# Optimization experiments

Hardware: AMD Instinct MI355X
Metric: run time of the kernel (lower is better)

## Reference

```python
import jax, jax.numpy as jnp
import numpy as np

NUM_NODES = 5000
NUM_COLORS = 20
NODE_FEAT = 4
COLOR_FEAT = 3
COMBINED = NODE_FEAT + COLOR_FEAT  # 7
HIDDEN = 128
N_GRAPH = NUM_NODES * NUM_COLORS   # 100000 GCN nodes (batch=1)
N_EDGES = 1_600_000


def setup_inputs() -> dict:
    key = jax.random.key(0)
    ks = jax.random.split(key, 12)
    flat_obs = jax.random.normal(ks[0], (1, 3 + NUM_NODES * NODE_FEAT + NUM_COLORS * COLOR_FEAT), dtype=jnp.float32)
    edge_index = jax.random.randint(ks[1], (2, N_EDGES), 0, N_GRAPH, dtype=jnp.int64)
    s = lambda k, sh, fan: jax.random.normal(k, sh, dtype=jnp.float32) / np.sqrt(fan)
    return {
        "flat_obs": flat_obs,
        "edge_index": edge_index,
        "W1": s(ks[2], (COMBINED, HIDDEN), COMBINED),
        "b1": jnp.zeros((HIDDEN,), jnp.float32),
        "W2": s(ks[3], (HIDDEN, HIDDEN), HIDDEN),
        "b2": jnp.zeros((HIDDEN,), jnp.float32),
        "fc1_w": s(ks[4], (HIDDEN, HIDDEN), HIDDEN),
        "fc1_b": jnp.zeros((HIDDEN,), jnp.float32),
        "fc2_w": s(ks[5], (HIDDEN, 1), HIDDEN),
        "fc2_b": jnp.zeros((1,), jnp.float32),
    }


def _gcn_conv(x, W, b, src, dst, norm):
    # PyG GCNConv: out[dst] += norm * (x @ W)[src]; self-loops already in src/dst.
    xw = x @ W                                   # [N, H]
    msg = xw[src] * norm[:, None]                # [E+N, H]
    out = jax.ops.segment_sum(msg, dst, num_segments=N_GRAPH)
    return out + b


def reference(flat_obs, edge_index, W1, b1, W2, b2, fc1_w, fc1_b, fc2_w, fc2_b):
    B = flat_obs.shape[0]
    nf_start = 3
    nf_end = nf_start + NUM_NODES * NODE_FEAT
    cf_end = nf_end + NUM_COLORS * COLOR_FEAT
    node_features = flat_obs[:, nf_start:nf_end].reshape(B, NUM_NODES, NODE_FEAT)
    color_features = flat_obs[:, nf_end:cf_end].reshape(B, NUM_COLORS, COLOR_FEAT)

    # cross-expand: [B, nodes, colors, 4+3]
    en = jnp.broadcast_to(node_features[:, :, None, :], (B, NUM_NODES, NUM_COLORS, NODE_FEAT))
    ec = jnp.broadcast_to(color_features[:, None, :, :], (B, NUM_NODES, NUM_COLORS, COLOR_FEAT))
    combined = jnp.concatenate([en, ec], axis=3).reshape(-1, COMBINED)  # [N_GRAPH, 7]

    # add self loops + symmetric normalization (GCN)
    loops = jnp.arange(N_GRAPH, dtype=edge_index.dtype)
    src = jnp.concatenate([edge_index[0], loops])
    dst = jnp.concatenate([edge_index[1], loops])
    deg = jax.ops.segment_sum(jnp.ones_like(dst, dtype=jnp.float32), dst, num_segments=N_GRAPH)
    dinv = jnp.where(deg > 0, jax.lax.rsqrt(deg), 0.0)
    norm = dinv[src] * dinv[dst]

    x = jax.nn.relu(_gcn_conv(combined, W1, b1, src, dst, norm))
    x = jax.nn.relu(_gcn_conv(x, W2, b2, src, dst, norm))
    x = jax.nn.relu(x @ fc1_w + fc1_b)
    q = x @ fc2_w + fc2_b                         # [N_GRAPH, 1]
    return q.reshape(B, NUM_NODES * NUM_COLORS)
```

## Files before the change

### kernel.cpp

```cpp
#include <hip/hip_runtime.h>
#include <hip/hip_fp16.h>

#define NGRAPH 100000
#define NEDGE  1600000
#define HID    128
#define SCAN_B 512
#define NBLK   ((NGRAPH + SCAN_B - 1) / SCAN_B)
#define TILE   64

__device__ __forceinline__ int e_src(const int* ei, int is64, int e) {
    return is64 ? ei[2 * e] : ei[e];
}
__device__ __forceinline__ int e_dst(const int* ei, int is64, int e) {
    return is64 ? ei[2 * NEDGE + 2 * e] : ei[NEDGE + e];
}

__global__ void k_prep(const float* __restrict__ obs, const int* __restrict__ ei,
                       float* __restrict__ comb, int* __restrict__ deg,
                       int* __restrict__ fill, int* __restrict__ flag) {
    if (blockIdx.x == 0 && threadIdx.x < 64) {
        int v = ei[2 * threadIdx.x + 1];
        unsigned long long b = __ballot(v != 0);
        if (threadIdx.x == 0) flag[0] = (b == 0ull) ? 1 : 0;
    }
    int i = blockIdx.x * blockDim.x + threadIdx.x;
    if (i >= NGRAPH) return;
    int n = i / 20, c = i % 20;
    const float* nf = obs + 3 + n * 4;
    const float* cf = obs + 3 + 20000 + c * 3;
    float* o = comb + i * 7;
    o[0] = nf[0]; o[1] = nf[1]; o[2] = nf[2]; o[3] = nf[3];
    o[4] = cf[0]; o[5] = cf[1]; o[6] = cf[2];
    deg[i] = 0;
    fill[i] = 0;
}

__global__ void k_deg(const int* __restrict__ ei, const int* __restrict__ flag,
                      int* __restrict__ deg) {
    int e = blockIdx.x * blockDim.x + threadIdx.x;
    if (e >= NEDGE) return;
    atomicAdd(&deg[e_dst(ei, flag[0], e)], 1);
}

__global__ void __launch_bounds__(SCAN_B) k_scan1(const int* __restrict__ deg,
                                                  int* __restrict__ rowptr,
                                                  int* __restrict__ sums,
                                                  float* __restrict__ dinv) {
    __shared__ int sh[SCAN_B];
    int t = threadIdx.x;
    int i = blockIdx.x * SCAN_B + t;
    int val = (i < NGRAPH) ? deg[i] : 0;
    if (i < NGRAPH) dinv[i] = rsqrtf((float)(val + 1));
    sh[t] = val;
    __syncthreads();
    for (int o = 1; o < SCAN_B; o <<= 1) {
        int x = (t >= o) ? sh[t - o] : 0;
        __syncthreads();
        sh[t] += x;
        __syncthreads();
    }
    if (i < NGRAPH) rowptr[i] = sh[t] - val;
    if (t == SCAN_B - 1) sums[blockIdx.x] = sh[t];
}

__global__ void __launch_bounds__(256) k_scan2(int* __restrict__ sums) {
    __shared__ int sh[256];
    int t = threadIdx.x;
    int val = (t < NBLK) ? sums[t] : 0;
    sh[t] = val;
    __syncthreads();
    for (int o = 1; o < 256; o <<= 1) {
        int x = (t >= o) ? sh[t - o] : 0;
        __syncthreads();
        sh[t] += x;
        __syncthreads();
    }
    if (t < NBLK) sums[t] = sh[t] - val;
}

__global__ void __launch_bounds__(SCAN_B) k_scan3(int* __restrict__ rowptr,
                                                  const int* __restrict__ sums) {
    int i = blockIdx.x * SCAN_B + threadIdx.x;
    if (i < NGRAPH) rowptr[i] += sums[blockIdx.x];
}

__global__ void k_fill(const int* __restrict__ ei, const int* __restrict__ flag,
                       const float* __restrict__ dinv,
                       const int* __restrict__ rowptr, int* __restrict__ fill,
                       int2* __restrict__ csr) {
    int e = blockIdx.x * blockDim.x + threadIdx.x;
    if (e >= NEDGE) return;
    int is64 = flag[0];
    int s = e_src(ei, is64, e);
    int d = e_dst(ei, is64, e);
    int pos = rowptr[d] + atomicAdd(&fill[d], 1);
    csr[pos] = make_int2(s, __float_as_int(dinv[s] * dinv[d]));
}

__global__ void __launch_bounds__(256) k_gcn1(const int* __restrict__ rowptr,
                                              const int* __restrict__ deg,
                                              const int2* __restrict__ csr,
                                              const float* __restrict__ dinv,
                                              const float* __restrict__ comb,
                                              const float* __restrict__ W1,
                                              const float* __restrict__ b1,
                                              __half* __restrict__ x1) {
    __shared__ float agg_s[32][8];
    int g = threadIdx.x >> 3;
    int f = threadIdx.x & 7;
    int d = blockIdx.x * 32 + g;
    if (f < 7) {
        int start = rowptr[d], n = deg[d];
        float acc = 0.0f;
        for (int j = 0; j < n; ++j) {
            int2 ed = csr[start + j];
            acc += __int_as_float(ed.y) * comb[ed.x * 7 + f];
        }
        float dv = dinv[d];
        acc += dv * dv * comb[d * 7 + f];
        agg_s[g][f] = acc;
    }
    __syncthreads();
    float a[7];
    #pragma unroll
    for (int q = 0; q < 7; ++q) a[q] = agg_s[g][q];
    int h0 = f * 16;
    #pragma unroll
    for (int j = 0; j < 4; ++j) {
        int h = h0 + j * 4;
        float4 acc4 = *reinterpret_cast<const float4*>(b1 + h);
        #pragma unroll
        for (int q = 0; q < 7; ++q) {
            float4 w = *reinterpret_cast<const float4*>(W1 + q * HID + h);
            acc4.x = fmaf(a[q], w.x, acc4.x);
            acc4.y = fmaf(a[q], w.y, acc4.y);
            acc4.z = fmaf(a[q], w.z, acc4.z);
            acc4.w = fmaf(a[q], w.w, acc4.w);
        }
        __half2 h01 = __floats2half2_rn(fmaxf(acc4.x, 0.0f), fmaxf(acc4.y, 0.0f));
        __half2 h23 = __floats2half2_rn(fmaxf(acc4.z, 0.0f), fmaxf(acc4.w, 0.0f));
        uint2 pk;
        pk.x = *reinterpret_cast<unsigned int*>(&h01);
        pk.y = *reinterpret_cast<unsigned int*>(&h23);
        *reinterpret_cast<uint2*>(x1 + (size_t)d * HID + h) = pk;
    }
}

__global__ void __launch_bounds__(256) k_agg2(const int* __restrict__ rowptr,
                                              const int* __restrict__ deg,
                                              const int2* __restrict__ csr,
                                              const float* __restrict__ dinv,
                                              const __half2* __restrict__ x1,
                                              float* __restrict__ agg2) {
    int wave = threadIdx.x >> 6;
    int lane = threadIdx.x & 63;
    int d = blockIdx.x * 4 + wave;
    int f0 = lane * 2;
    int start = rowptr[d], n = deg[d];
    float2 acc = {0.0f, 0.0f};
    int j = 0;
    for (; j + 2 <= n; j += 2) {
        int2 e0 = csr[start + j];
        int2 e1 = csr[start + j + 1];
        float w0 = __int_as_float(e0.y);
        float w1 = __int_as_float(e1.y);
        float2 v0 = __half22float2(x1[(size_t)e0.x * 64 + lane]);
        float2 v1 = __half22float2(x1[(size_t)e1.x * 64 + lane]);
        acc.x = fmaf(w0, v0.x, acc.x);
        acc.y = fmaf(w0, v0.y, acc.y);
        acc.x = fmaf(w1, v1.x, acc.x);
        acc.y = fmaf(w1, v1.y, acc.y);
    }
    if (j < n) {
        int2 e0 = csr[start + j];
        float w0 = __int_as_float(e0.y);
        float2 v0 = __half22float2(x1[(size_t)e0.x * 64 + lane]);
        acc.x = fmaf(w0, v0.x, acc.x);
        acc.y = fmaf(w0, v0.y, acc.y);
    }
    float dv = dinv[d];
    float ws = dv * dv;
    float2 v = __half22float2(x1[(size_t)d * 64 + lane]);
    acc.x = fmaf(ws, v.x, acc.x);
    acc.y = fmaf(ws, v.y, acc.y);
    *reinterpret_cast<float2*>(agg2 + (size_t)d * HID + f0) = acc;
}

__device__ __forceinline__ void fmad(float4& acc, float s, const float4 w) {
    acc.x = fmaf(s, w.x, acc.x);
    acc.y = fmaf(s, w.y, acc.y);
    acc.z = fmaf(s, w.z, acc.z);
    acc.w = fmaf(s, w.w, acc.w);
}
__device__ __forceinline__ float4 relu4(float4 v) {
    float4 r;
    r.x = fmaxf(v.x, 0.0f); r.y = fmaxf(v.y, 0.0f);
    r.z = fmaxf(v.z, 0.0f); r.w = fmaxf(v.w, 0.0f);
    return r;
}

__global__ void __launch_bounds__(256, 3) k_mlp(const float* __restrict__ agg2,
                                                const float* __restrict__ W2,
                                                const float* __restrict__ b2,
                                                const float* __restrict__ fc1w,
                                                const float* __restrict__ fc1b,
                                                const float* __restrict__ fc2w,
                                                const float* __restrict__ fc2b,
                                                float* __restrict__ out) {
    __shared__ float as_[TILE][HID + 4];
    __shared__ float ws[32][HID + 4];
    const int tid = threadIdx.x;
    const int tx = tid & 15;
    const int ty = tid >> 4;
    const int n0 = blockIdx.x * TILE;
    const int hA = tx * 4;
    const int hB = 64 + tx * 4;

    #pragma unroll
    for (int q = 0; q < 8; ++q) {
        int idx = (q * 256 + tid) * 4;
        int row = idx >> 7, col = idx & 127;
        int nr = n0 + row; if (nr >= NGRAPH) nr = NGRAPH - 1;
        *reinterpret_cast<float4*>(&as_[row][col]) =
            *reinterpret_cast<const float4*>(agg2 + (size_t)nr * HID + col);
    }

    float4 cA[4], cB[4];
    {
        float4 bA = *reinterpret_cast<const float4*>(b2 + hA);
        float4 bB = *reinterpret_cast<const float4*>(b2 + hB);
        #pragma unroll
        for (int r = 0; r < 4; ++r) { cA[r] = bA; cB[r] = bB; }
    }
    for (int ks = 0; ks < HID; ks += 32) {
        #pragma unroll
        for (int q = 0; q < 4; ++q) {
            int idx = (q * 256 + tid) * 4;
            int row = idx >> 7, col = idx & 127;
            *reinterpret_cast<float4*>(&ws[row][col]) =
                *reinterpret_cast<const float4*>(W2 + (size_t)(ks + row) * HID + col);
        }
        __syncthreads();
        #pragma unroll
        for (int k = 0; k < 32; k += 4) {
            float4 wA0 = *reinterpret_cast<const float4*>(&ws[k + 0][hA]);
            float4 wB0 = *reinterpret_cast<const float4*>(&ws[k + 0][hB]);
            float4 wA1 = *reinterpret_cast<const float4*>(&ws[k + 1][hA]);
            float4 wB1 = *reinterpret_cast<const float4*>(&ws[k + 1][hB]);
            float4 wA2 = *reinterpret_cast<const float4*>(&ws[k + 2][hA]);
            float4 wB2 = *reinterpret_cast<const float4*>(&ws[k + 2][hB]);
            float4 wA3 = *reinterpret_cast<const float4*>(&ws[k + 3][hA]);
            float4 wB3 = *reinterpret_cast<const float4*>(&ws[k + 3][hB]);
            #pragma unroll
            for (int r = 0; r < 4; ++r) {
                float4 a = *reinterpret_cast<const float4*>(&as_[ty * 4 + r][ks + k]);
                fmad(cA[r], a.x, wA0); fmad(cB[r], a.x, wB0);
                fmad(cA[r], a.y, wA1); fmad(cB[r], a.y, wB1);
                fmad(cA[r], a.z, wA2); fmad(cB[r], a.z, wB2);
                fmad(cA[r], a.w, wA3); fmad(cB[r], a.w, wB3);
            }
        }
        __syncthreads();
    }
    #pragma unroll
    for (int r = 0; r < 4; ++r) {
        *reinterpret_cast<float4*>(&as_[ty * 4 + r][hA]) = relu4(cA[r]);
        *reinterpret_cast<float4*>(&as_[ty * 4 + r][hB]) = relu4(cB[r]);
    }

    float4 dA[4], dB[4];
    {
        float4 bA = *reinterpret_cast<const float4*>(fc1b + hA);
        float4 bB = *reinterpret_cast<const float4*>(fc1b + hB);
        #pragma unroll
        for (int r = 0; r < 4; ++r) { dA[r] = bA; dB[r] = bB; }
    }
    for (int ks = 0; ks < HID; ks += 32) {
        #pragma unroll
        for (int q = 0; q < 4; ++q) {
            int idx = (q * 256 + tid) * 4;
            int row = idx >> 7, col = idx & 127;
            *reinterpret_cast<float4*>(&ws[row][col]) =
                *reinterpret_cast<const float4*>(fc1w + (size_t)(ks + row) * HID + col);
        }
        __syncthreads();
        #pragma unroll
        for (int k = 0; k < 32; k += 4) {
            float4 wA0 = *reinterpret_cast<const float4*>(&ws[k + 0][hA]);
            float4 wB0 = *reinterpret_cast<const float4*>(&ws[k + 0][hB]);
            float4 wA1 = *reinterpret_cast<const float4*>(&ws[k + 1][hA]);
            float4 wB1 = *reinterpret_cast<const float4*>(&ws[k + 1][hB]);
            float4 wA2 = *reinterpret_cast<const float4*>(&ws[k + 2][hA]);
            float4 wB2 = *reinterpret_cast<const float4*>(&ws[k + 2][hB]);
            float4 wA3 = *reinterpret_cast<const float4*>(&ws[k + 3][hA]);
            float4 wB3 = *reinterpret_cast<const float4*>(&ws[k + 3][hB]);
            #pragma unroll
            for (int r = 0; r < 4; ++r) {
                float4 a = *reinterpret_cast<const float4*>(&as_[ty * 4 + r][ks + k]);
                fmad(dA[r], a.x, wA0); fmad(dB[r], a.x, wB0);
                fmad(dA[r], a.y, wA1); fmad(dB[r], a.y, wB1);
                fmad(dA[r], a.z, wA2); fmad(dB[r], a.z, wB2);
                fmad(dA[r], a.w, wA3); fmad(dB[r], a.w, wB3);
            }
        }
        __syncthreads();
    }

    float4 wqA = *reinterpret_cast<const float4*>(fc2w + hA);
    float4 wqB = *reinterpret_cast<const float4*>(fc2w + hB);
    float p[4];
    #pragma unroll
    for (int r = 0; r < 4; ++r) {
        float4 rA = relu4(dA[r]);
        float4 rB = relu4(dB[r]);
        p[r] = rA.x * wqA.x + rA.y * wqA.y + rA.z * wqA.z + rA.w * wqA.w
             + rB.x * wqB.x + rB.y * wqB.y + rB.z * wqB.z + rB.w * wqB.w;
    }
    #pragma unroll
    for (int m = 1; m < 16; m <<= 1) {
        #pragma unroll
        for (int r = 0; r < 4; ++r) p[r] += __shfl_xor(p[r], m);
    }
    if (tx == 0) {
        float bq = fc2b[0];
        int nb = n0 + ty * 4;
        #pragma unroll
        for (int r = 0; r < 4; ++r)
            if (nb + r < NGRAPH) out[nb + r] = p[r] + bq;
    }
}

extern "C" void kernel_launch(void* const* d_in, const int* in_sizes, int n_in,
                              void* d_out, int out_size, void* d_ws, size_t ws_size,
                              hipStream_t stream) {
    const float* obs  = (const float*)d_in[0];
    const int*   ei   = (const int*)d_in[1];
    const float* W1   = (const float*)d_in[2];
    const float* b1   = (const float*)d_in[3];
    const float* W2   = (const float*)d_in[4];
    const float* b2   = (const float*)d_in[5];
    const float* fc1w = (const float*)d_in[6];
    const float* fc1b = (const float*)d_in[7];
    const float* fc2w = (const float*)d_in[8];
    const float* fc2b = (const float*)d_in[9];
    float* out = (float*)d_out;

    char* base = (char*)d_ws;
    size_t off = 0;
    auto take = [&](size_t bytes) {
        char* p = base + off;
        off += (bytes + 255) & ~(size_t)255;
        return p;
    };
    int*    deg     = (int*)take((size_t)NGRAPH * 4);
    int*    rowptr  = (int*)take((size_t)NGRAPH * 4);
    int*    fill    = (int*)take((size_t)NGRAPH * 4);
    int*    sums    = (int*)take((size_t)NBLK * 4);
    float*  dinv    = (float*)take((size_t)NGRAPH * 4);
    int2*   csr     = (int2*)take((size_t)NEDGE * 8);
    float*  comb    = (float*)take((size_t)NGRAPH * 7 * 4);
    __half* x1      = (__half*)take((size_t)NGRAPH * HID * 2);
    float*  agg2    = (float*)take((size_t)NGRAPH * HID * 4);
    int*    flag    = (int*)take(256);

    k_prep<<<(NGRAPH + 255) / 256, 256, 0, stream>>>(obs, ei, comb, deg, fill, flag);
    k_deg<<<(NEDGE + 255) / 256, 256, 0, stream>>>(ei, flag, deg);
    k_scan1<<<NBLK, SCAN_B, 0, stream>>>(deg, rowptr, sums, dinv);
    k_scan2<<<1, 256, 0, stream>>>(sums);
    k_scan3<<<NBLK, SCAN_B, 0, stream>>>(rowptr, sums);
    k_fill<<<(NEDGE + 255) / 256, 256, 0, stream>>>(ei, flag, dinv, rowptr, fill, csr);
    k_gcn1<<<NGRAPH / 32, 256, 0, stream>>>(rowptr, deg, csr, dinv,
                                            comb, W1, b1, x1);
    k_agg2<<<NGRAPH / 4, 256, 0, stream>>>(rowptr, deg, csr, dinv,
                                           (const __half2*)x1, agg2);
    k_mlp<<<(NGRAPH + TILE - 1) / TILE, 256, 0, stream>>>(agg2, W2, b2,
                                                          fc1w, fc1b,
                                                          fc2w, fc2b, out);
}
```

Measured before the change: 460.8 us.

## Use fill pointers for CSR build, unroll gathers, change LDS padding

The scan writes an absolute fill pointer per node, so the CSR fill pass needs one atomic per edge and no longer reads rowptr separately. The separate zeroing of the fill counters is removed. The gather loops in the two aggregation kernels are unrolled (2x in gcn1, 4x in agg2) so more independent loads are in flight. The MLP shared-memory row padding changes from +4 to +2 floats. That changes bank-conflict behaviour and may misalign float4 accesses into LDS.

```diff
diff --git a/kernel.cpp b/kernel.cpp
--- a/kernel.cpp
+++ b/kernel.cpp
@@ -7,6 +7,7 @@
 #define SCAN_B 512
 #define NBLK   ((NGRAPH + SCAN_B - 1) / SCAN_B)
 #define TILE   64
+#define LPAD   (HID + 2)
 
 __device__ __forceinline__ int e_src(const int* ei, int is64, int e) {
     return is64 ? ei[2 * e] : ei[e];
@@ -17,7 +18,7 @@
 
 __global__ void k_prep(const float* __restrict__ obs, const int* __restrict__ ei,
                        float* __restrict__ comb, int* __restrict__ deg,
-                       int* __restrict__ fill, int* __restrict__ flag) {
+                       int* __restrict__ flag) {
     if (blockIdx.x == 0 && threadIdx.x < 64) {
         int v = ei[2 * threadIdx.x + 1];
         unsigned long long b = __ballot(v != 0);
@@ -32,7 +33,6 @@
     o[0] = nf[0]; o[1] = nf[1]; o[2] = nf[2]; o[3] = nf[3];
     o[4] = cf[0]; o[5] = cf[1]; o[6] = cf[2];
     deg[i] = 0;
-    fill[i] = 0;
 }
 
 __global__ void k_deg(const int* __restrict__ ei, const int* __restrict__ flag,
@@ -79,21 +79,25 @@
 }
 
 __global__ void __launch_bounds__(SCAN_B) k_scan3(int* __restrict__ rowptr,
-                                                  const int* __restrict__ sums) {
+                                                  const int* __restrict__ sums,
+                                                  int* __restrict__ fillptr) {
     int i = blockIdx.x * SCAN_B + threadIdx.x;
-    if (i < NGRAPH) rowptr[i] += sums[blockIdx.x];
+    if (i < NGRAPH) {
+        int v = rowptr[i] + sums[blockIdx.x];
+        rowptr[i] = v;
+        fillptr[i] = v;
+    }
 }
 
 __global__ void k_fill(const int* __restrict__ ei, const int* __restrict__ flag,
                        const float* __restrict__ dinv,
-                       const int* __restrict__ rowptr, int* __restrict__ fill,
-                       int2* __restrict__ csr) {
+                       int* __restrict__ fillptr, int2* __restrict__ csr) {
     int e = blockIdx.x * blockDim.x + threadIdx.x;
     if (e >= NEDGE) return;
     int is64 = flag[0];
     int s = e_src(ei, is64, e);
     int d = e_dst(ei, is64, e);
-    int pos = rowptr[d] + atomicAdd(&fill[d], 1);
+    int pos = atomicAdd(&fillptr[d], 1);
     csr[pos] = make_int2(s, __float_as_int(dinv[s] * dinv[d]));
 }
 
@@ -112,12 +116,21 @@
     if (f < 7) {
         int start = rowptr[d], n = deg[d];
         float acc = 0.0f;
-        for (int j = 0; j < n; ++j) {
-            int2 ed = csr[start + j];
-            acc += __int_as_float(ed.y) * comb[ed.x * 7 + f];
+        int j = 0;
+        for (; j + 2 <= n; j += 2) {
+            int2 e0 = csr[start + j];
+            int2 e1 = csr[start + j + 1];
+            float c0 = comb[e0.x * 7 + f];
+            float c1 = comb[e1.x * 7 + f];
+            acc = fmaf(__int_as_float(e0.y), c0, acc);
+            acc = fmaf(__int_as_float(e1.y), c1, acc);
+        }
+        if (j < n) {
+            int2 e0 = csr[start + j];
+            acc = fmaf(__int_as_float(e0.y), comb[e0.x * 7 + f], acc);
         }
         float dv = dinv[d];
-        acc += dv * dv * comb[d * 7 + f];
+        acc = fmaf(dv * dv, comb[d * 7 + f], acc);
         agg_s[g][f] = acc;
     }
     __syncthreads();
@@ -159,24 +172,29 @@
     int start = rowptr[d], n = deg[d];
     float2 acc = {0.0f, 0.0f};
     int j = 0;
-    for (; j + 2 <= n; j += 2) {
+    for (; j + 4 <= n; j += 4) {
         int2 e0 = csr[start + j];
         int2 e1 = csr[start + j + 1];
-        float w0 = __int_as_float(e0.y);
-        float w1 = __int_as_float(e1.y);
+        int2 e2 = csr[start + j + 2];
+        int2 e3 = csr[start + j + 3];
         float2 v0 = __half22float2(x1[(size_t)e0.x * 64 + lane]);
         float2 v1 = __half22float2(x1[(size_t)e1.x * 64 + lane]);
-        acc.x = fmaf(w0, v0.x, acc.x);
-        acc.y = fmaf(w0, v0.y, acc.y);
-        acc.x = fmaf(w1, v1.x, acc.x);
-        acc.y = fmaf(w1, v1.y, acc.y);
-    }
-    if (j < n) {
+        float2 v2 = __half22float2(x1[(size_t)e2.x * 64 + lane]);
+        float2 v3 = __half22float2(x1[(size_t)e3.x * 64 + lane]);
+        acc.x = fmaf(__int_as_float(e0.y), v0.x, acc.x);
+        acc.y = fmaf(__int_as_float(e0.y), v0.y, acc.y);
+        acc.x = fmaf(__int_as_float(e1.y), v1.x, acc.x);
+        acc.y = fmaf(__int_as_float(e1.y), v1.y, acc.y);
+        acc.x = fmaf(__int_as_float(e2.y), v2.x, acc.x);
+        acc.y = fmaf(__int_as_float(e2.y), v2.y, acc.y);
+        acc.x = fmaf(__int_as_float(e3.y), v3.x, acc.x);
+        acc.y = fmaf(__int_as_float(e3.y), v3.y, acc.y);
+    }
+    for (; j < n; ++j) {
         int2 e0 = csr[start + j];
-        float w0 = __int_as_float(e0.y);
         float2 v0 = __half22float2(x1[(size_t)e0.x * 64 + lane]);
-        acc.x = fmaf(w0, v0.x, acc.x);
-        acc.y = fmaf(w0, v0.y, acc.y);
+        acc.x = fmaf(__int_as_float(e0.y), v0.x, acc.x);
+        acc.y = fmaf(__int_as_float(e0.y), v0.y, acc.y);
     }
     float dv = dinv[d];
     float ws = dv * dv;
@@ -207,8 +225,8 @@
                                                 const float* __restrict__ fc2w,
                                                 const float* __restrict__ fc2b,
                                                 float* __restrict__ out) {
-    __shared__ float as_[TILE][HID + 4];
-    __shared__ float ws[32][HID + 4];
+    __shared__ float as_[TILE][LPAD];
+    __shared__ float ws[32][LPAD];
     const int tid = threadIdx.x;
     const int tx = tid & 15;
     const int ty = tid >> 4;
@@ -354,7 +372,7 @@
     };
     int*    deg     = (int*)take((size_t)NGRAPH * 4);
     int*    rowptr  = (int*)take((size_t)NGRAPH * 4);
-    int*    fill    = (int*)take((size_t)NGRAPH * 4);
+    int*    fillptr = (int*)take((size_t)NGRAPH * 4);
     int*    sums    = (int*)take((size_t)NBLK * 4);
     float*  dinv    = (float*)take((size_t)NGRAPH * 4);
     int2*   csr     = (int2*)take((size_t)NEDGE * 8);
@@ -363,12 +381,12 @@
     float*  agg2    = (float*)take((size_t)NGRAPH * HID * 4);
     int*    flag    = (int*)take(256);
 
-    k_prep<<<(NGRAPH + 255) / 256, 256, 0, stream>>>(obs, ei, comb, deg, fill, flag);
+    k_prep<<<(NGRAPH + 255) / 256, 256, 0, stream>>>(obs, ei, comb, deg, flag);
     k_deg<<<(NEDGE + 255) / 256, 256, 0, stream>>>(ei, flag, deg);
     k_scan1<<<NBLK, SCAN_B, 0, stream>>>(deg, rowptr, sums, dinv);
     k_scan2<<<1, 256, 0, stream>>>(sums);
-    k_scan3<<<NBLK, SCAN_B, 0, stream>>>(rowptr, sums);
-    k_fill<<<(NEDGE + 255) / 256, 256, 0, stream>>>(ei, flag, dinv, rowptr, fill, csr);
+    k_scan3<<<NBLK, SCAN_B, 0, stream>>>(rowptr, sums, fillptr);
+    k_fill<<<(NEDGE + 255) / 256, 256, 0, stream>>>(ei, flag, dinv, fillptr, csr);
     k_gcn1<<<NGRAPH / 32, 256, 0, stream>>>(rowptr, deg, csr, dinv,
                                             comb, W1, b1, x1);
     k_agg2<<<NGRAPH / 4, 256, 0, stream>>>(rowptr, deg, csr, dinv,
```

Measured after the change: 450.1 us. 2.3% less time.
